# Performance work log

Hardware: AMD Instinct MI355X
Metric: run time of the kernel (lower is better)

The kernel has to match this reference:

```python
import jax, jax.numpy as jnp
import numpy as np

ROPE_BASE = 10000.0
NEG_INF = -1e30

def _apply_rope(x):
    # x: [B, H, T, D]; interleaved-pair RoPE (torchtune style), positions along axis -2.
    B, H, T, D = x.shape
    inv_freq = 1.0 / (ROPE_BASE ** (jnp.arange(0, D, 2, dtype=jnp.float32) / D))  # [D/2]
    ang = jnp.arange(T, dtype=jnp.float32)[:, None] * inv_freq[None, :]           # [T, D/2]
    cos, sin = jnp.cos(ang), jnp.sin(ang)
    x1, x2 = x[..., 0::2], x[..., 1::2]                                           # [B,H,T,D/2]
    rot = jnp.stack([x1 * cos - x2 * sin, x1 * sin + x2 * cos], axis=-1)          # [B,H,T,D/2,2]
    return rot.reshape(B, H, T, D).astype(x.dtype)

def setup_inputs() -> dict:
    key = jax.random.key(0)
    ks = jax.random.split(key, 5)
    B, T, C = 2, 2048, 1024
    s = 1.0 / np.sqrt(C)
    return {
        "x":  jax.random.normal(ks[0], (B, T, C), jnp.float32),
        "Wq": jax.random.normal(ks[1], (C, C), jnp.float32) * s,
        "bq": jnp.zeros((C,), jnp.float32),
        "Wk": jax.random.normal(ks[2], (C, C), jnp.float32) * s,
        "bk": jnp.zeros((C,), jnp.float32),
        "Wv": jax.random.normal(ks[3], (C, C), jnp.float32) * s,
        "bv": jnp.zeros((C,), jnp.float32),
        "Wo": jax.random.normal(ks[4], (C, C), jnp.float32) * s,
        "bo": jnp.zeros((C,), jnp.float32),
    }

def reference(x, Wq, bq, Wk, bk, Wv, bv, Wo, bo):
    B, T, C = x.shape
    H = 16
    D = C // H
    # QKV projections (torch Linear: x @ W.T + b), split heads -> [B, H, T, D]
    def proj(W, b):
        return (jnp.einsum('btc,oc->bto', x, W) + b).reshape(B, T, H, D).transpose(0, 2, 1, 3)
    q = _apply_rope(proj(Wq, bq))
    k = _apply_rope(proj(Wk, bk))
    v = proj(Wv, bv)
    # Causal scaled dot-product attention
    scale = 1.0 / jnp.sqrt(jnp.asarray(D, x.dtype))
    scores = jnp.einsum('bhqd,bhkd->bhqk', q, k) * scale                          # [B,H,T,T]
    causal = jnp.tril(jnp.ones((T, T), dtype=bool))
    scores = jnp.where(causal, scores, NEG_INF)
    probs = jax.nn.softmax(scores, axis=-1)
    y = jnp.einsum('bhqk,bhkd->bhqd', probs, v)                                   # [B,H,T,D]
    y = y.transpose(0, 2, 1, 3).reshape(B, T, C)
    # Output projection (dropout is identity in eval mode)
    return jnp.einsum('btc,oc->bto', y, Wo) + bo
```

## Files before the change

### kernel.cpp

```cpp
#include <hip/hip_runtime.h>

#define BB 2
#define TT 2048
#define CC 1024
#define HH 16
#define DD 64
#define KDIM 1024
#define MROWS (BB*TT)

typedef __attribute__((ext_vector_type(8))) short  frag_b16;
typedef __attribute__((ext_vector_type(4))) float  f32x4;
typedef __attribute__((ext_vector_type(4))) unsigned short us4;
typedef __attribute__((ext_vector_type(8))) unsigned short us8;
typedef __attribute__((ext_vector_type(4))) _Float16 f16x4;
typedef __attribute__((ext_vector_type(8))) _Float16 f16x8;

#define EXP2F(x) __builtin_amdgcn_exp2f(x)

__device__ __forceinline__ unsigned short f2bf(float f) {
    unsigned int u = __builtin_bit_cast(unsigned int, f);
    u += 0x7FFFu + ((u >> 16) & 1u);
    return (unsigned short)(u >> 16);
}

__device__ __forceinline__ void gl_lds16(const void* g, void* l) {
    __builtin_amdgcn_global_load_lds(
        (const __attribute__((address_space(1))) unsigned int*)g,
        (__attribute__((address_space(3))) unsigned int*)l, 16, 0, 0);
}

__global__ __launch_bounds__(256) void cvt_all(
        const float* __restrict__ x,  const float* __restrict__ w0,
        const float* __restrict__ w1, const float* __restrict__ w2,
        const float* __restrict__ w3, unsigned short* __restrict__ dst) {
    const size_t NX = (size_t)MROWS * CC;
    const size_t NW = (size_t)CC * CC;
    size_t i = ((size_t)blockIdx.x * 256 + threadIdx.x) * 4;
    const float* src; size_t off;
    if (i < NX) { src = x; off = i; }
    else {
        size_t j = i - NX;
        int t = (int)(j >> 20);
        src = (t == 0) ? w0 : (t == 1) ? w1 : (t == 2) ? w2 : w3;
        off = j & (NW - 1);
    }
    float4 f = *reinterpret_cast<const float4*>(src + off);
    us4 o;
    o.x = f2bf(f.x); o.y = f2bf(f.y); o.z = f2bf(f.z); o.w = f2bf(f.w);
    *reinterpret_cast<us4*>(dst + i) = o;
}

__global__ __launch_bounds__(256, 3) void qkv_gemm_rope(
        const unsigned short* __restrict__ X,
        const unsigned short* __restrict__ Wq,
        const unsigned short* __restrict__ Wk,
        const unsigned short* __restrict__ Wv,
        const float* __restrict__ bq, const float* __restrict__ bk,
        const float* __restrict__ bv,
        unsigned short* __restrict__ Qo,
        unsigned short* __restrict__ Ko,
        _Float16* __restrict__ VTo)
{
    const int z = blockIdx.z;
    const unsigned short* W = (z == 0) ? Wq : (z == 1) ? Wk : Wv;
    const float* bias = (z == 0) ? bq : (z == 1) ? bk : bv;

    const int tid = threadIdx.x;
    const int wave = tid >> 6;
    const int lane = tid & 63;
    const int l16 = lane & 15;
    const int quad = lane >> 4;

    const int bx = blockIdx.x * 128;
    const int by = blockIdx.y * 128;
    const int row0 = bx + (wave >> 1) * 64;
    const int col0 = by + (wave & 1) * 64;

    __shared__ __align__(16) char smem[36864];
    unsigned short (*Xa)[32] = (unsigned short(*)[32])smem;
    unsigned short (*Wb)[32] = (unsigned short(*)[32])(smem + 8192);
    _Float16 (*Vl)[64][72] = (_Float16(*)[64][72])smem;

    f32x4 acc[4][4] = {};

    const int c0 = tid, c1 = tid + 256;
    const int r0s = c0 >> 2, o0s = (c0 & 3) * 8;
    const int r1s = c1 >> 2, o1s = (c1 & 3) * 8;

    for (int kk = 0; kk < KDIM; kk += 32) {
        gl_lds16(X + (size_t)(bx + r0s) * KDIM + kk + o0s, (unsigned short*)Xa + c0 * 8);
        gl_lds16(X + (size_t)(bx + r1s) * KDIM + kk + o1s, (unsigned short*)Xa + c1 * 8);
        gl_lds16(W + (size_t)(by + r0s) * KDIM + kk + o0s, (unsigned short*)Wb + c0 * 8);
        gl_lds16(W + (size_t)(by + r1s) * KDIM + kk + o1s, (unsigned short*)Wb + c1 * 8);
        __syncthreads();

        frag_b16 a[4], b[4];
#pragma unroll
        for (int r = 0; r < 4; ++r)
            a[r] = *reinterpret_cast<const frag_b16*>(
                &Xa[(wave >> 1) * 64 + r * 16 + l16][quad * 8]);
#pragma unroll
        for (int c = 0; c < 4; ++c)
            b[c] = *reinterpret_cast<const frag_b16*>(
                &Wb[(wave & 1) * 64 + c * 16 + l16][quad * 8]);
#pragma unroll
        for (int r = 0; r < 4; ++r)
#pragma unroll
            for (int c = 0; c < 4; ++c)
                acc[r][c] = __builtin_amdgcn_mfma_f32_16x16x32_bf16(a[r], b[c], acc[r][c], 0, 0, 0);
        __syncthreads();
    }

    if (z == 2) {
#pragma unroll
        for (int r = 0; r < 4; ++r)
#pragma unroll
            for (int c = 0; c < 4; ++c) {
                f16x4 pk;
#pragma unroll
                for (int g = 0; g < 4; ++g)
                    pk[g] = (_Float16)(acc[r][c][g] + bias[col0 + c * 16 + l16]);
                *reinterpret_cast<f16x4*>(&Vl[wave][c * 16 + l16][r * 16 + quad * 4]) = pk;
            }
        const int b_ = row0 >> 11;
        const int t_base = row0 & (TT - 1);
        const int h = col0 >> 6;
        const int dl = lane >> 3;
        const int t8 = (lane & 7) * 8;
        __builtin_amdgcn_s_waitcnt(0);
#pragma unroll
        for (int i = 0; i < 8; ++i) {
            int d = i * 8 + dl;
            f16x8 v = *reinterpret_cast<const f16x8*>(&Vl[wave][d][t8]);
            *reinterpret_cast<f16x8*>(
                &VTo[((size_t)(b_ * HH + h) * DD + d) * TT + t_base + t8]) = v;
        }
    } else {
        const float qsc = (z == 0) ? 0.180336888f : 1.0f;
        unsigned short* dst = (z == 0) ? Qo : Ko;
        const int b_ = row0 >> 11;
        const int tq0 = (row0 & (TT - 1)) + quad * 4;
#pragma unroll
        for (int c = 0; c < 4; ++c) {
            const int o = col0 + c * 16 + l16;
            const int h = o >> 6, d = o & (DD - 1);
            const float inv = __expf(-(float)(d & ~1) * (9.210340371976184f / (float)DD));
            float cs0, sn0, cs1, sn1, cs16, sn16;
            __sincosf((float)tq0 * inv, &sn0, &cs0);
            __sincosf(inv, &sn1, &cs1);
            __sincosf(16.f * inv, &sn16, &cs16);
            float cr = cs0, sr = sn0;
#pragma unroll
            for (int r = 0; r < 4; ++r) {
                float cg = cr, sg = sr;
#pragma unroll
                for (int g = 0; g < 4; ++g) {
                    int n = row0 + r * 16 + quad * 4 + g;
                    int t = n & (TT - 1);
                    float v = acc[r][c][g] + bias[o];
                    float pv = __shfl_xor(v, 1);
                    float outv = (d & 1) ? (pv * sg + v * cg) : (v * cg - pv * sg);
                    dst[((size_t)(b_ * HH + h) * TT + t) * DD + d] = f2bf(outv * qsc);
                    float cn = cg * cs1 - sg * sn1;
                    sg = sg * cs1 + cg * sn1;
                    cg = cn;
                }
                float crn = cr * cs16 - sr * sn16;
                sr = sr * cs16 + cr * sn16;
                cr = crn;
            }
        }
    }
}

__global__ __launch_bounds__(256, 2) void attn(
        const unsigned short* __restrict__ Q,
        const unsigned short* __restrict__ K,
        const _Float16* __restrict__ VT,
        unsigned short* __restrict__ Y)
{
    const int b1d = blockIdx.x;
    const int bh = (b1d & 7) * 4 + ((b1d >> 3) & 3);
    const int pair = b1d >> 5;
    const int tid = threadIdx.x;
    const int w = tid >> 6;
    const int lane = tid & 63;
    const int l16 = lane & 15;
    const int quad = lane >> 4;

    const unsigned short* Qp = Q + (size_t)bh * TT * DD;
    const unsigned short* Kp = K + (size_t)bh * TT * DD;
    const _Float16* Vp = VT + (size_t)bh * DD * TT;

    __shared__ unsigned short Kl[2][128][64];
    __shared__ _Float16 Vl[2][64][128];
    __shared__ unsigned short Ylds[4][16][72];

    const int sw = (l16 & 7);
    const int b_ = bh >> 4, h = bh & (HH - 1);

    f16x4 ones;
    ones[0] = ones[1] = ones[2] = ones[3] = (_Float16)1.0f;

#pragma unroll 1
    for (int seg = 0; seg < 2; ++seg) {
        const int qblk = seg ? (31 - pair) : pair;
        const int q0 = qblk * 64;
        const int q = q0 + w * 16 + l16;

        frag_b16 bq[2];
#pragma unroll
        for (int dk = 0; dk < 2; ++dk)
            bq[dk] = *reinterpret_cast<const frag_b16*>(
                Qp + (size_t)q * DD + dk * 32 + quad * 8);

        f32x4 yacc[4] = {};
        f32x4 lsum = {};

        const int ntiles = (qblk >> 1) + 1;

#pragma unroll
        for (int i = 0; i < 4; ++i) {
            int n = tid + 256 * i;
            int kr = n >> 3,  kc = ((n & 7)  ^ (kr & 7)) * 8;
            int vr = n >> 4,  vc = ((n & 15) ^ (vr & 7)) * 8;
            gl_lds16(Kp + (size_t)kr * DD + kc, (unsigned short*)&Kl[0][0][0] + n * 8);
            gl_lds16(Vp + (size_t)vr * TT + vc, (_Float16*)&Vl[0][0][0] + n * 8);
        }

#pragma unroll 1
        for (int it = 0; it < ntiles; ++it) {
            __syncthreads();
            const int bsel = it & 1;
            if (it + 1 < ntiles) {
                const int jn = (it + 1) * 128;
                const int bn = bsel ^ 1;
#pragma unroll
                for (int i = 0; i < 4; ++i) {
                    int n = tid + 256 * i;
                    int kr = n >> 3,  kc = ((n & 7)  ^ (kr & 7)) * 8;
                    int vr = n >> 4,  vc = ((n & 15) ^ (vr & 7)) * 8;
                    gl_lds16(Kp + (size_t)(jn + kr) * DD + kc,
                             (unsigned short*)&Kl[bn][0][0] + n * 8);
                    gl_lds16(Vp + (size_t)vr * TT + jn + vc,
                             (_Float16*)&Vl[bn][0][0] + n * 8);
                }
            }
            const int j0 = it * 128;

            f32x4 s[8];
#pragma unroll
            for (int mt = 0; mt < 8; ++mt) {
                frag_b16 ak0 = *reinterpret_cast<const frag_b16*>(
                    &Kl[bsel][mt * 16 + l16][(quad ^ sw) * 8]);
                frag_b16 ak1 = *reinterpret_cast<const frag_b16*>(
                    &Kl[bsel][mt * 16 + l16][((4 + quad) ^ sw) * 8]);
                f32x4 t = {};
                t = __builtin_amdgcn_mfma_f32_16x16x32_bf16(ak0, bq[0], t, 0, 0, 0);
                t = __builtin_amdgcn_mfma_f32_16x16x32_bf16(ak1, bq[1], t, 0, 0, 0);
                s[mt] = t;
            }

            if (it == ntiles - 1) {
#pragma unroll
                for (int mt = 0; mt < 8; ++mt)
#pragma unroll
                    for (int g = 0; g < 4; ++g) {
                        int key = j0 + mt * 16 + quad * 4 + g;
                        if (key > q) s[mt][g] = -1e30f;
                    }
            }

            f16x4 pb[8];
#pragma unroll
            for (int mt = 0; mt < 8; ++mt)
#pragma unroll
                for (int g = 0; g < 4; ++g)
                    pb[mt][g] = (_Float16)EXP2F(s[mt][g] - 11.0f);

#pragma unroll
            for (int kt = 0; kt < 8; ++kt)
                lsum = __builtin_amdgcn_mfma_f32_16x16x16f16(ones, pb[kt], lsum, 0, 0, 0);

#pragma unroll
            for (int dt = 0; dt < 4; ++dt) {
                f32x4 ya = yacc[dt];
#pragma unroll
                for (int kt = 0; kt < 8; ++kt) {
                    int colp = (kt * 2 + (quad >> 1)) ^ sw;
                    f16x4 av = *reinterpret_cast<const f16x4*>(
                        &Vl[bsel][dt * 16 + l16][colp * 8 + (quad & 1) * 4]);
                    ya = __builtin_amdgcn_mfma_f32_16x16x16f16(av, pb[kt], ya, 0, 0, 0);
                }
                yacc[dt] = ya;
            }
        }

        __syncthreads();

        float rl = 1.f / lsum[0];
#pragma unroll
        for (int dt = 0; dt < 4; ++dt)
#pragma unroll
            for (int g = 0; g < 4; ++g)
                Ylds[w][l16][dt * 16 + quad * 4 + g] = f2bf(yacc[dt][g] * rl);

#pragma unroll
        for (int i = 0; i < 2; ++i) {
            int idx = i * 64 + lane;
            int r = idx >> 3, c8 = (idx & 7) * 8;
            us8 v = *reinterpret_cast<const us8*>(&Ylds[w][r][c8]);
            *reinterpret_cast<us8*>(
                &Y[(size_t)(b_ * TT + q0 + w * 16 + r) * CC + h * DD + c8]) = v;
        }
    }
}

__global__ __launch_bounds__(256, 2) void out_gemm(
        const unsigned short* __restrict__ Y,
        const unsigned short* __restrict__ Wo,
        const float* __restrict__ bo,
        float* __restrict__ out)
{
    const int tid = threadIdx.x;
    const int wave = tid >> 6;
    const int lane = tid & 63;
    const int l16 = lane & 15;
    const int quad = lane >> 4;

    const int bx = blockIdx.x * 128;
    const int by = blockIdx.y * 128;
    const int row0 = bx + (wave >> 1) * 64;
    const int col0 = by + (wave & 1) * 64;

    __shared__ unsigned short Xa[128][32];
    __shared__ unsigned short Wb[128][32];

    f32x4 acc[4][4] = {};

    const int c0 = tid, c1 = tid + 256;
    const int r0s = c0 >> 2, o0s = (c0 & 3) * 8;
    const int r1s = c1 >> 2, o1s = (c1 & 3) * 8;

    for (int kk = 0; kk < KDIM; kk += 32) {
        gl_lds16(Y  + (size_t)(bx + r0s) * KDIM + kk + o0s, (unsigned short*)Xa + c0 * 8);
        gl_lds16(Y  + (size_t)(bx + r1s) * KDIM + kk + o1s, (unsigned short*)Xa + c1 * 8);
        gl_lds16(Wo + (size_t)(by + r0s) * KDIM + kk + o0s, (unsigned short*)Wb + c0 * 8);
        gl_lds16(Wo + (size_t)(by + r1s) * KDIM + kk + o1s, (unsigned short*)Wb + c1 * 8);
        __syncthreads();

        frag_b16 a[4], b[4];
#pragma unroll
        for (int r = 0; r < 4; ++r)
            a[r] = *reinterpret_cast<const frag_b16*>(
                &Xa[(wave >> 1) * 64 + r * 16 + l16][quad * 8]);
#pragma unroll
        for (int c = 0; c < 4; ++c)
            b[c] = *reinterpret_cast<const frag_b16*>(
                &Wb[(wave & 1) * 64 + c * 16 + l16][quad * 8]);
#pragma unroll
        for (int r = 0; r < 4; ++r)
#pragma unroll
            for (int c = 0; c < 4; ++c)
                acc[r][c] = __builtin_amdgcn_mfma_f32_16x16x32_bf16(a[r], b[c], acc[r][c], 0, 0, 0);
        __syncthreads();
    }

#pragma unroll
    for (int r = 0; r < 4; ++r)
#pragma unroll
        for (int c = 0; c < 4; ++c)
#pragma unroll
            for (int g = 0; g < 4; ++g) {
                int n = row0 + r * 16 + quad * 4 + g;
                int o = col0 + c * 16 + l16;
                out[(size_t)n * CC + o] = acc[r][c][g] + bo[o];
            }
}

extern "C" void kernel_launch(void* const* d_in, const int* in_sizes, int n_in,
                              void* d_out, int out_size, void* d_ws, size_t ws_size,
                              hipStream_t stream) {
    const float* x  = (const float*)d_in[0];
    const float* Wq = (const float*)d_in[1];
    const float* bq = (const float*)d_in[2];
    const float* Wk = (const float*)d_in[3];
    const float* bk = (const float*)d_in[4];
    const float* Wv = (const float*)d_in[5];
    const float* bv = (const float*)d_in[6];
    const float* Wo = (const float*)d_in[7];
    const float* bo = (const float*)d_in[8];
    float* out = (float*)d_out;

    unsigned short* ws = (unsigned short*)d_ws;
    const size_t NX = (size_t)MROWS * CC;
    const size_t NW = (size_t)CC * CC;
    unsigned short* xb  = ws;
    unsigned short* wqb = xb  + NX;
    unsigned short* wkb = wqb + NW;
    unsigned short* wvb = wkb + NW;
    unsigned short* wob = wvb + NW;
    unsigned short* Qr  = wob + NW;
    unsigned short* Kr  = Qr  + NX;
    _Float16*       VTb = (_Float16*)(Kr + NX);
    unsigned short* Yb  = (unsigned short*)(VTb + NX);

    const size_t NALL = NX + 4 * NW;
    cvt_all<<<dim3((unsigned)(NALL / 1024)), 256, 0, stream>>>(x, Wq, Wk, Wv, Wo, xb);

    qkv_gemm_rope<<<dim3(MROWS / 128, CC / 128, 3), 256, 0, stream>>>(
        xb, wqb, wkb, wvb, bq, bk, bv, Qr, Kr, VTb);

    attn<<<dim3(512), 256, 0, stream>>>(Qr, Kr, VTb, Yb);

    out_gemm<<<dim3(MROWS / 128, CC / 128), 256, 0, stream>>>(Yb, wob, bo, out);
}
```

Measured before the change: 179.2 us.

## Double-buffer GEMM K-loop with 64-wide K tiles and XOR-swizzled LDS

Rewrites the K-loop of the QKV and output projection GEMMs to use two LDS buffers, so the global-to-LDS load of the next 64-wide K tile overlaps the MFMA work on the current tile. K steps drop from 32 to 16, and each step needs one barrier instead of two. LDS rows are XOR-swizzled to avoid bank conflicts on fragment reads. LDS per block grows to 64 KB and the QKV kernel's occupancy bound drops from 3 to 2 blocks, which may reduce latency hiding.

```diff
diff --git a/kernel.cpp b/kernel.cpp
--- a/kernel.cpp
+++ b/kernel.cpp
@@ -50,7 +50,7 @@
     *reinterpret_cast<us4*>(dst + i) = o;
 }
 
-__global__ __launch_bounds__(256, 3) void qkv_gemm_rope(
+__global__ __launch_bounds__(256, 2) void qkv_gemm_rope(
         const unsigned short* __restrict__ X,
         const unsigned short* __restrict__ Wq,
         const unsigned short* __restrict__ Wk,
@@ -76,40 +76,79 @@
     const int row0 = bx + (wave >> 1) * 64;
     const int col0 = by + (wave & 1) * 64;
 
-    __shared__ __align__(16) char smem[36864];
-    unsigned short (*Xa)[32] = (unsigned short(*)[32])smem;
-    unsigned short (*Wb)[32] = (unsigned short(*)[32])(smem + 8192);
+    __shared__ __align__(16) char smem[65536];
+    unsigned short* Xa0 = (unsigned short*)smem;
+    unsigned short* Wb0 = (unsigned short*)(smem + 32768);
     _Float16 (*Vl)[64][72] = (_Float16(*)[64][72])smem;
 
     f32x4 acc[4][4] = {};
 
-    const int c0 = tid, c1 = tid + 256;
-    const int r0s = c0 >> 2, o0s = (c0 & 3) * 8;
-    const int r1s = c1 >> 2, o1s = (c1 & 3) * 8;
-
-    for (int kk = 0; kk < KDIM; kk += 32) {
-        gl_lds16(X + (size_t)(bx + r0s) * KDIM + kk + o0s, (unsigned short*)Xa + c0 * 8);
-        gl_lds16(X + (size_t)(bx + r1s) * KDIM + kk + o1s, (unsigned short*)Xa + c1 * 8);
-        gl_lds16(W + (size_t)(by + r0s) * KDIM + kk + o0s, (unsigned short*)Wb + c0 * 8);
-        gl_lds16(W + (size_t)(by + r1s) * KDIM + kk + o1s, (unsigned short*)Wb + c1 * 8);
+    int srow[4]; int scol[4];
+#pragma unroll
+    for (int i = 0; i < 4; ++i) {
+        int n = tid + 256 * i;
+        srow[i] = n >> 3;
+        scol[i] = ((n & 7) ^ (srow[i] & 7)) * 8;
+    }
+
+#pragma unroll
+    for (int i = 0; i < 4; ++i) {
+        int n = tid + 256 * i;
+        gl_lds16(X + (size_t)(bx + srow[i]) * KDIM + scol[i], Xa0 + n * 8);
+        gl_lds16(W + (size_t)(by + srow[i]) * KDIM + scol[i], Wb0 + n * 8);
+    }
+
+    const int ar = (wave >> 1) * 64;
+    const int bc = (wave & 1) * 64;
+
+#pragma unroll 1
+    for (int step = 0; step < 16; ++step) {
         __syncthreads();
-
-        frag_b16 a[4], b[4];
+        const int bsel = step & 1;
+        if (step + 1 < 16) {
+            const int kk = (step + 1) * 64;
+            const int bo_ = (bsel ^ 1) * 8192;
+#pragma unroll
+            for (int i = 0; i < 4; ++i) {
+                int n = tid + 256 * i;
+                gl_lds16(X + (size_t)(bx + srow[i]) * KDIM + kk + scol[i],
+                         Xa0 + bo_ + n * 8);
+                gl_lds16(W + (size_t)(by + srow[i]) * KDIM + kk + scol[i],
+                         Wb0 + bo_ + n * 8);
+            }
+        }
+
+        frag_b16 a[4][2], b[4][2];
+#pragma unroll
+        for (int r = 0; r < 4; ++r) {
+            int row = ar + r * 16 + l16;
+#pragma unroll
+            for (int kh = 0; kh < 2; ++kh) {
+                int c = (kh * 4 + quad) ^ (row & 7);
+                a[r][kh] = *reinterpret_cast<const frag_b16*>(
+                    Xa0 + bsel * 8192 + row * 64 + c * 8);
+            }
+        }
+#pragma unroll
+        for (int cc = 0; cc < 4; ++cc) {
+            int row = bc + cc * 16 + l16;
+#pragma unroll
+            for (int kh = 0; kh < 2; ++kh) {
+                int c = (kh * 4 + quad) ^ (row & 7);
+                b[cc][kh] = *reinterpret_cast<const frag_b16*>(
+                    Wb0 + bsel * 8192 + row * 64 + c * 8);
+            }
+        }
 #pragma unroll
         for (int r = 0; r < 4; ++r)
-            a[r] = *reinterpret_cast<const frag_b16*>(
-                &Xa[(wave >> 1) * 64 + r * 16 + l16][quad * 8]);
-#pragma unroll
-        for (int c = 0; c < 4; ++c)
-            b[c] = *reinterpret_cast<const frag_b16*>(
-                &Wb[(wave & 1) * 64 + c * 16 + l16][quad * 8]);
-#pragma unroll
-        for (int r = 0; r < 4; ++r)
-#pragma unroll
-            for (int c = 0; c < 4; ++c)
-                acc[r][c] = __builtin_amdgcn_mfma_f32_16x16x32_bf16(a[r], b[c], acc[r][c], 0, 0, 0);
-        __syncthreads();
-    }
+#pragma unroll
+            for (int c = 0; c < 4; ++c) {
+                acc[r][c] = __builtin_amdgcn_mfma_f32_16x16x32_bf16(a[r][0], b[c][0], acc[r][c], 0, 0, 0);
+                acc[r][c] = __builtin_amdgcn_mfma_f32_16x16x32_bf16(a[r][1], b[c][1], acc[r][c], 0, 0, 0);
+            }
+    }
+
+    __syncthreads();
 
     if (z == 2) {
 #pragma unroll
@@ -333,37 +372,75 @@
     const int row0 = bx + (wave >> 1) * 64;
     const int col0 = by + (wave & 1) * 64;
 
-    __shared__ unsigned short Xa[128][32];
-    __shared__ unsigned short Wb[128][32];
+    __shared__ __align__(16) char smem[65536];
+    unsigned short* Xa0 = (unsigned short*)smem;
+    unsigned short* Wb0 = (unsigned short*)(smem + 32768);
 
     f32x4 acc[4][4] = {};
 
-    const int c0 = tid, c1 = tid + 256;
-    const int r0s = c0 >> 2, o0s = (c0 & 3) * 8;
-    const int r1s = c1 >> 2, o1s = (c1 & 3) * 8;
-
-    for (int kk = 0; kk < KDIM; kk += 32) {
-        gl_lds16(Y  + (size_t)(bx + r0s) * KDIM + kk + o0s, (unsigned short*)Xa + c0 * 8);
-        gl_lds16(Y  + (size_t)(bx + r1s) * KDIM + kk + o1s, (unsigned short*)Xa + c1 * 8);
-        gl_lds16(Wo + (size_t)(by + r0s) * KDIM + kk + o0s, (unsigned short*)Wb + c0 * 8);
-        gl_lds16(Wo + (size_t)(by + r1s) * KDIM + kk + o1s, (unsigned short*)Wb + c1 * 8);
+    int srow[4]; int scol[4];
+#pragma unroll
+    for (int i = 0; i < 4; ++i) {
+        int n = tid + 256 * i;
+        srow[i] = n >> 3;
+        scol[i] = ((n & 7) ^ (srow[i] & 7)) * 8;
+    }
+
+#pragma unroll
+    for (int i = 0; i < 4; ++i) {
+        int n = tid + 256 * i;
+        gl_lds16(Y  + (size_t)(bx + srow[i]) * KDIM + scol[i], Xa0 + n * 8);
+        gl_lds16(Wo + (size_t)(by + srow[i]) * KDIM + scol[i], Wb0 + n * 8);
+    }
+
+    const int ar = (wave >> 1) * 64;
+    const int bc = (wave & 1) * 64;
+
+#pragma unroll 1
+    for (int step = 0; step < 16; ++step) {
         __syncthreads();
-
-        frag_b16 a[4], b[4];
+        const int bsel = step & 1;
+        if (step + 1 < 16) {
+            const int kk = (step + 1) * 64;
+            const int bo_ = (bsel ^ 1) * 8192;
+#pragma unroll
+            for (int i = 0; i < 4; ++i) {
+                int n = tid + 256 * i;
+                gl_lds16(Y  + (size_t)(bx + srow[i]) * KDIM + kk + scol[i],
+                         Xa0 + bo_ + n * 8);
+                gl_lds16(Wo + (size_t)(by + srow[i]) * KDIM + kk + scol[i],
+                         Wb0 + bo_ + n * 8);
+            }
+        }
+
+        frag_b16 a[4][2], b[4][2];
+#pragma unroll
+        for (int r = 0; r < 4; ++r) {
+            int row = ar + r * 16 + l16;
+#pragma unroll
+            for (int kh = 0; kh < 2; ++kh) {
+                int c = (kh * 4 + quad) ^ (row & 7);
+                a[r][kh] = *reinterpret_cast<const frag_b16*>(
+                    Xa0 + bsel * 8192 + row * 64 + c * 8);
+            }
+        }
+#pragma unroll
+        for (int cc = 0; cc < 4; ++cc) {
+            int row = bc + cc * 16 + l16;
+#pragma unroll
+            for (int kh = 0; kh < 2; ++kh) {
+                int c = (kh * 4 + quad) ^ (row & 7);
+                b[cc][kh] = *reinterpret_cast<const frag_b16*>(
+                    Wb0 + bsel * 8192 + row * 64 + c * 8);
+            }
+        }
 #pragma unroll
         for (int r = 0; r < 4; ++r)
-            a[r] = *reinterpret_cast<const frag_b16*>(
-                &Xa[(wave >> 1) * 64 + r * 16 + l16][quad * 8]);
-#pragma unroll
-        for (int c = 0; c < 4; ++c)
-            b[c] = *reinterpret_cast<const frag_b16*>(
-                &Wb[(wave & 1) * 64 + c * 16 + l16][quad * 8]);
-#pragma unroll
-        for (int r = 0; r < 4; ++r)
-#pragma unroll
-            for (int c = 0; c < 4; ++c)
-                acc[r][c] = __builtin_amdgcn_mfma_f32_16x16x32_bf16(a[r], b[c], acc[r][c], 0, 0, 0);
-        __syncthreads();
+#pragma unroll
+            for (int c = 0; c < 4; ++c) {
+                acc[r][c] = __builtin_amdgcn_mfma_f32_16x16x32_bf16(a[r][0], b[c][0], acc[r][c], 0, 0, 0);
+                acc[r][c] = __builtin_amdgcn_mfma_f32_16x16x32_bf16(a[r][1], b[c][1], acc[r][c], 0, 0, 0);
+            }
     }
 
 #pragma unroll
```

Measured after the change: 175.6 us. -2.0%, faster.
